# Kernel tuning notes

Hardware: AMD Instinct MI355X
Metric: run time of the kernel (lower is better)

## Reference

```python
import jax, jax.numpy as jnp
import numpy as np

NEG_SLOPE = 0.2


def _gat_layer(x, edge_index, W, a_src, a_dst, b):
    """PyG GATConv: linear -> per-edge attention logits -> segment softmax over
    destination -> scatter-add weighted messages. Self-loops added (PyG default)."""
    N = x.shape[0]
    heads, out = a_src.shape
    loops = jnp.arange(N, dtype=edge_index.dtype)
    src = jnp.concatenate([edge_index[0], loops])
    dst = jnp.concatenate([edge_index[1], loops])
    xh = (x @ W).reshape(N, heads, out)                      # [N,H,D]
    alpha_s = (xh * a_src).sum(-1)                           # [N,H]
    alpha_d = (xh * a_dst).sum(-1)                           # [N,H]
    e = jax.nn.leaky_relu(alpha_s[src] + alpha_d[dst], NEG_SLOPE)  # [E,H]
    emax = jax.ops.segment_max(e, dst, num_segments=N)       # [N,H]
    ex = jnp.exp(e - emax[dst])
    den = jax.ops.segment_sum(ex, dst, num_segments=N)
    att = ex / (den[dst] + 1e-16)                            # [E,H]
    msg = xh[src] * att[..., None]                           # [E,H,D]
    o = jax.ops.segment_sum(msg, dst, num_segments=N)        # [N,H,D]
    return o.reshape(N, heads * out) + b


def _single_source_gnn(h, edge_index, params):
    n_layers = len(params)
    for i, (W, a_s, a_d, b) in enumerate(params):
        h = _gat_layer(h, edge_index, W, a_s, a_d, b)
        if i < n_layers - 1:
            h = jax.nn.relu(h)
    return h


def setup_inputs() -> dict:
    key = jax.random.key(0)
    B, N, H, heads, deg = 4, 2000, 64, 4, 32
    E = N * deg
    ks = jax.random.split(key, 20)

    def mk_edge_index(k):
        e = jax.random.randint(k, (2, B, E), 0, N)
        off = (jnp.arange(B) * N)[None, :, None]
        return (e + off).reshape(2, B * E).astype(jnp.int32)

    inp = {
        "h0_flat": jax.random.normal(ks[0], (B * N, H), jnp.float32),
        "edge_index_s1": mk_edge_index(ks[1]),
        "edge_index_s2": mk_edge_index(ks[2]),
    }
    dims = [(H, H * heads), (H * heads, H * heads)]
    i = 3
    for s in ("s1", "s2"):
        for l, (din, dout) in enumerate(dims):
            inp[f"W_{s}_{l}"] = jax.random.normal(ks[i], (din, dout), jnp.float32) * 0.1; i += 1
            inp[f"a_src_{s}_{l}"] = jax.random.normal(ks[i], (heads, H), jnp.float32) * 0.1; i += 1
            inp[f"a_dst_{s}_{l}"] = jax.random.normal(ks[i], (heads, H), jnp.float32) * 0.1; i += 1
            inp[f"b_{s}_{l}"] = jnp.zeros((dout,), jnp.float32)
    inp["batch_size"] = B
    inp["num_stocks"] = N
    return inp


def reference(h0_flat, edge_index_s1, edge_index_s2,
              W_s1_0, a_src_s1_0, a_dst_s1_0, b_s1_0,
              W_s1_1, a_src_s1_1, a_dst_s1_1, b_s1_1,
              W_s2_0, a_src_s2_0, a_dst_s2_0, b_s2_0,
              W_s2_1, a_src_s2_1, a_dst_s2_1, b_s2_1,
              batch_size, num_stocks):
    p1 = [(W_s1_0, a_src_s1_0, a_dst_s1_0, b_s1_0),
          (W_s1_1, a_src_s1_1, a_dst_s1_1, b_s1_1)]
    p2 = [(W_s2_0, a_src_s2_0, a_dst_s2_0, b_s2_0),
          (W_s2_1, a_src_s2_1, a_dst_s2_1, b_s2_1)]
    h1 = _single_source_gnn(h0_flat, edge_index_s1, p1)
    h2 = _single_source_gnn(h0_flat, edge_index_s2, p2)
    # dict of per-source outputs in torch -> stacked [n_sources, B*N, H*heads]
    return jnp.stack([h1, h2])
```

## Files before the change

kernel.cpp:

```cpp
#include <hip/hip_runtime.h>
#include <hip/hip_fp16.h>


#define NEG_SLOPE 0.2f
#define ELLW 96
#define BK 64
#define HPAD 8

typedef _Float16 half8 __attribute__((ext_vector_type(8)));
typedef float floatx4 __attribute__((ext_vector_type(4)));

struct Args {
    const float* h0;
    const int *ei1, *ei2;
    const float *W10, *W11, *W20, *W21;
    const float *as10, *ad10, *b10, *as11, *ad11, *b11;
    const float *as20, *ad20, *b20, *as21, *ad21, *b21;
    _Float16 *Wt10, *Wt20, *Wt11, *Wt21;
    int *cnt, *slots;
    _Float16 *xh1, *xh2;
    _Float16 *hb1, *hb2;
    float *alS1, *alD1, *alS2, *alD2;
    float *out0, *out1;
    int N, E1, E2, GB0;
};


__global__ __launch_bounds__(64) void wt_zero_kernel(Args a) {
    int z = blockIdx.z, y = blockIdx.y, c = blockIdx.x;
    int t = threadIdx.x;
    int flat = ((z * gridDim.y + y) * gridDim.x + c) * 64 + t;
    if (flat < 2 * a.N) a.cnt[flat] = 0;
    if (y == 0) {
        const float* W  = z ? a.W20  : a.W10;
        _Float16*    Wt = z ? a.Wt20 : a.Wt10;
        Wt[(size_t)c * 64 + t] = (_Float16)W[(size_t)t * 256 + c];
    } else {
        int k = (y - 1) * 64 + t;
        const float* W  = z ? a.W21  : a.W11;
        _Float16*    Wt = z ? a.Wt21 : a.Wt11;
        Wt[(size_t)c * 256 + k] = (_Float16)W[(size_t)k * 256 + c];
    }
}


template<bool AHALF>
__device__ __forceinline__ void gemm_tile(
        const void* hv, const _Float16* __restrict__ Wt,
        const float* __restrict__ a_s, const float* __restrict__ a_d,
        _Float16* __restrict__ xh, float* __restrict__ alS,
        float* __restrict__ alD, int K, int row0,
        _Float16 (&hT)[32][BK + HPAD]) {
    int tid  = threadIdx.x;
    int wave = tid >> 6;
    int lane = tid & 63;
    int lo = lane & 15, hi = lane >> 4;
    int c0 = wave * 64;

    floatx4 acc[2][4] = {};

    int srow = tid >> 3, sseg = tid & 7;
    const _Float16* wbase = Wt + (size_t)c0 * K;

    for (int k0 = 0; k0 < K; k0 += BK) {
        __syncthreads();
        if (AHALF) {
            const _Float16* hrow = (const _Float16*)hv
                                 + (size_t)(row0 + srow) * K + sseg * 8;
            *(half8*)&hT[srow][sseg * 8] = *(const half8*)(hrow + k0);
        } else {
            const float* hrow = (const float*)hv
                              + (size_t)(row0 + srow) * K + sseg * 8;
            float4 hv0 = *(const float4*)(hrow + k0);
            float4 hv1 = *(const float4*)(hrow + k0 + 4);
            half8 hh;
            hh[0] = (_Float16)hv0.x; hh[1] = (_Float16)hv0.y;
            hh[2] = (_Float16)hv0.z; hh[3] = (_Float16)hv0.w;
            hh[4] = (_Float16)hv1.x; hh[5] = (_Float16)hv1.y;
            hh[6] = (_Float16)hv1.z; hh[7] = (_Float16)hv1.w;
            *(half8*)&hT[srow][sseg * 8] = hh;
        }
        __syncthreads();

        half8 bf[2][4], af[2][2];
#pragma unroll
        for (int ks = 0; ks < 2; ks++) {
#pragma unroll
            for (int cf = 0; cf < 4; cf++)
                bf[ks][cf] = *(const half8*)(wbase + (size_t)(cf * 16 + lo) * K
                                             + k0 + ks * 32 + hi * 8);
#pragma unroll
            for (int f = 0; f < 2; f++)
                af[ks][f] = *(const half8*)&hT[f * 16 + lo][ks * 32 + hi * 8];
        }
#pragma unroll
        for (int ks = 0; ks < 2; ks++)
#pragma unroll
            for (int f = 0; f < 2; f++)
#pragma unroll
                for (int cf = 0; cf < 4; cf++)
                    acc[f][cf] = __builtin_amdgcn_mfma_f32_16x16x32_f16(
                        af[ks][f], bf[ks][cf], acc[f][cf], 0, 0, 0);
    }

    float asw[4], adw[4];
#pragma unroll
    for (int cf = 0; cf < 4; cf++) {
        asw[cf] = a_s[c0 + cf * 16 + lo];
        adw[cf] = a_d[c0 + cf * 16 + lo];
    }
#pragma unroll
    for (int f = 0; f < 2; f++) {
#pragma unroll
        for (int r = 0; r < 4; r++) {
            int row = row0 + f * 16 + hi * 4 + r;
            float v0 = acc[f][0][r], v1 = acc[f][1][r];
            float v2 = acc[f][2][r], v3 = acc[f][3][r];
            _Float16* xrow = &xh[(size_t)row * 256 + c0 + lo];
            xrow[0]  = (_Float16)v0;
            xrow[16] = (_Float16)v1;
            xrow[32] = (_Float16)v2;
            xrow[48] = (_Float16)v3;
            float s1 = v0 * asw[0] + v1 * asw[1] + v2 * asw[2] + v3 * asw[3];
            float s2 = v0 * adw[0] + v1 * adw[1] + v2 * adw[2] + v3 * adw[3];
#pragma unroll
            for (int off = 1; off < 16; off <<= 1) {
                s1 += __shfl_xor(s1, off);
                s2 += __shfl_xor(s2, off);
            }
            if (lo == 0) {
                alS[row * 4 + wave] = s1;
                alD[row * 4 + wave] = s2;
            }
        }
    }
}


__global__ __launch_bounds__(256) void g0scat_kernel(Args a) {
    __shared__ _Float16 hT[32][BK + HPAD];
    int b = blockIdx.x;
    if (b < a.GB0) {
        int half_ = a.GB0 >> 1;
        int s = (b >= half_);
        int bx = b - s * half_;
        gemm_tile<false>(a.h0, s ? a.Wt20 : a.Wt10,
                         s ? a.as20 : a.as10, s ? a.ad20 : a.ad10,
                         s ? a.xh2 : a.xh1, s ? a.alS2 : a.alS1,
                         s ? a.alD2 : a.alD1, 64, bx * 32, hT);
    } else {
        int i = (b - a.GB0) * 256 + threadIdx.x;
        int tot1 = a.E1 + a.N, tot2 = a.E2 + a.N;
        if (i >= tot1 + tot2) return;
        int s, j; const int* ei; int E;
        if (i < tot1) { s = 0; j = i;        ei = a.ei1; E = a.E1; }
        else          { s = 1; j = i - tot1; ei = a.ei2; E = a.E2; }
        int src, dst;
        if (j < E) { src = ei[j]; dst = ei[E + j]; }
        else       { src = dst = j - E; }
        int gg = s * a.N + dst;
        int pos = atomicAdd(&a.cnt[gg], 1);
        if (pos < ELLW) a.slots[(size_t)gg * ELLW + pos] = src;
    }
}

__global__ __launch_bounds__(256) void gemm1_kernel(Args a) {
    __shared__ _Float16 hT[32][BK + HPAD];
    int half_ = a.GB0 >> 1;
    int b = blockIdx.x;
    int s = (b >= half_);
    int bx = b - s * half_;
    gemm_tile<true>(s ? a.hb2 : a.hb1, s ? a.Wt21 : a.Wt11,
                    s ? a.as21 : a.as11, s ? a.ad21 : a.ad11,
                    s ? a.xh2 : a.xh1, s ? a.alS2 : a.alS1,
                    s ? a.alD2 : a.alD1, 256, bx * 32, hT);
}


template<bool OUTHALF>
__device__ __forceinline__ void attn_impl(
        const Args& a, const float* __restrict__ b1, const float* __restrict__ b2,
        void* o1, void* o2, int do_relu) {
    __shared__ float2 pairs[4][8][10];
    int tid = threadIdx.x;
    int h = tid >> 6, L = tid & 63, st = L >> 3, lc = L & 7;
    int b = blockIdx.x;
    int cpx = (2 * a.N) >> 3;
    int g = (b & 7) * cpx + (b >> 3);
    int s = (g >= a.N) ? 1 : 0;
    int dst = g - s * a.N;
    const _Float16* xh  = s ? a.xh2  : a.xh1;
    const float*  alS   = s ? a.alS2 : a.alS1;
    const float*  alD   = s ? a.alD2 : a.alD1;
    const float*  bias  = s ? b2 : b1;
    void*         out   = s ? o2 : o1;

    const int* slots = a.slots + (size_t)g * ELLW;
    int pre = slots[L];
    int nd = a.cnt[g];
    if (nd > ELLW) nd = ELLW;
    float ad = alD[dst * 4 + h];
    const char* xb = (const char*)xh + h * 128 + lc * 16;

    float acc[8] = {};
    float pden = 0.f;

    for (int c = 0; c < nd; c += 64) {
        int n = nd - c; if (n > 64) n = 64;
        int off = 0; float p = 0.f;
        if (L < n) {
            int src = (c == 0) ? pre : slots[c + L];
            float t = alS[src * 4 + h] + ad;
            t = (t > 0.f) ? t : NEG_SLOPE * t;
            p = __expf(t);
            off = src * 512;
        }
        pden += p;
        pairs[h][L & 7][L >> 3] = make_float2(__int_as_float(off), p);
        int iters = (n + 7) >> 3;
        for (int ii = 0; ii < iters; ii += 4) {
            float4 twoA = *(const float4*)&pairs[h][st][ii];
            float4 twoB = *(const float4*)&pairs[h][st][ii + 2];
            int   o0 = __float_as_int(twoA.x); float w0 = twoA.y;
            int   o1i = __float_as_int(twoA.z); float w1 = twoA.w;
            int   o2i = __float_as_int(twoB.x); float w2 = twoB.y;
            int   o3i = __float_as_int(twoB.z); float w3 = twoB.w;
            float4 r0 = *(const float4*)(xb + o0);
            float4 r1 = *(const float4*)(xb + o1i);
            float4 r2 = *(const float4*)(xb + o2i);
            float4 r3 = *(const float4*)(xb + o3i);
            const __half2* q0 = (const __half2*)&r0;
            const __half2* q1 = (const __half2*)&r1;
            const __half2* q2 = (const __half2*)&r2;
            const __half2* q3 = (const __half2*)&r3;
#pragma unroll
            for (int k = 0; k < 4; k++) {
                acc[2 * k + 0] += (float)q0[k].x * w0;
                acc[2 * k + 1] += (float)q0[k].y * w0;
                acc[2 * k + 0] += (float)q1[k].x * w1;
                acc[2 * k + 1] += (float)q1[k].y * w1;
                acc[2 * k + 0] += (float)q2[k].x * w2;
                acc[2 * k + 1] += (float)q2[k].y * w2;
                acc[2 * k + 0] += (float)q3[k].x * w3;
                acc[2 * k + 1] += (float)q3[k].y * w3;
            }
        }
    }
#pragma unroll
    for (int k = 0; k < 8; k++) {
        acc[k] += __shfl_xor(acc[k], 8);
        acc[k] += __shfl_xor(acc[k], 16);
        acc[k] += __shfl_xor(acc[k], 32);
    }
#pragma unroll
    for (int o2_ = 32; o2_ >= 1; o2_ >>= 1) pden += __shfl_xor(pden, o2_);

    if (st == 0) {
        float d = 1.0f / (pden + 1e-16f);
        int col = h * 64 + lc * 8;
        float4 bA = *(const float4*)&bias[col];
        float4 bB = *(const float4*)&bias[col + 4];
        float o[8];
        o[0] = acc[0] * d + bA.x; o[1] = acc[1] * d + bA.y;
        o[2] = acc[2] * d + bA.z; o[3] = acc[3] * d + bA.w;
        o[4] = acc[4] * d + bB.x; o[5] = acc[5] * d + bB.y;
        o[6] = acc[6] * d + bB.z; o[7] = acc[7] * d + bB.w;
        if (do_relu) {
#pragma unroll
            for (int k = 0; k < 8; k++) o[k] = fmaxf(o[k], 0.f);
        }
        if (OUTHALF) {
            half8 ov;
#pragma unroll
            for (int k = 0; k < 8; k++) ov[k] = (_Float16)o[k];
            *(half8*)((_Float16*)out + (size_t)dst * 256 + col) = ov;
        } else {
            float4 oA, oB;
            oA.x = o[0]; oA.y = o[1]; oA.z = o[2]; oA.w = o[3];
            oB.x = o[4]; oB.y = o[5]; oB.z = o[6]; oB.w = o[7];
            *(float4*)((float*)out + (size_t)dst * 256 + col) = oA;
            *(float4*)((float*)out + (size_t)dst * 256 + col + 4) = oB;
        }
    }
}

__global__ __launch_bounds__(256) void attn0_kernel(Args a) {
    attn_impl<true>(a, a.b10, a.b20, a.hb1, a.hb2, 1);
}
__global__ __launch_bounds__(256) void attn1_kernel(Args a) {
    attn_impl<false>(a, a.b11, a.b21, a.out0, a.out1, 0);
}


extern "C" void kernel_launch(void* const* d_in, const int* in_sizes, int n_in,
                              void* d_out, int out_size, void* d_ws, size_t ws_size,
                              hipStream_t stream) {
    const int N  = in_sizes[0] / 64;
    const int E1 = in_sizes[1] / 2;
    const int E2 = in_sizes[2] / 2;

    char* base = (char*)d_ws;
    size_t off = 0;
    auto carve = [&](size_t bytes) -> void* {
        void* p = base + off;
        off += (bytes + 255) & ~(size_t)255;
        return p;
    };
    int* cnt        = (int*)carve((size_t)2 * N * 4);
    int* slots      = (int*)carve((size_t)2 * N * ELLW * 4);
    _Float16* xh1   = (_Float16*)carve((size_t)N * 256 * 2);
    _Float16* xh2   = (_Float16*)carve((size_t)N * 256 * 2);
    _Float16* hb1   = (_Float16*)carve((size_t)N * 256 * 2);
    _Float16* hb2   = (_Float16*)carve((size_t)N * 256 * 2);
    float* alS1     = (float*)carve((size_t)N * 4 * 4);
    float* alD1     = (float*)carve((size_t)N * 4 * 4);
    float* alS2     = (float*)carve((size_t)N * 4 * 4);
    float* alD2     = (float*)carve((size_t)N * 4 * 4);
    _Float16* Wt10  = (_Float16*)carve((size_t)256 * 64 * 2);
    _Float16* Wt20  = (_Float16*)carve((size_t)256 * 64 * 2);
    _Float16* Wt11  = (_Float16*)carve((size_t)256 * 256 * 2);
    _Float16* Wt21  = (_Float16*)carve((size_t)256 * 256 * 2);
    (void)ws_size; (void)n_in;

    Args a;
    a.h0 = (const float*)d_in[0];
    a.ei1 = (const int*)d_in[1];
    a.ei2 = (const int*)d_in[2];
    a.W10 = (const float*)d_in[3];  a.as10 = (const float*)d_in[4];
    a.ad10 = (const float*)d_in[5]; a.b10 = (const float*)d_in[6];
    a.W11 = (const float*)d_in[7];  a.as11 = (const float*)d_in[8];
    a.ad11 = (const float*)d_in[9]; a.b11 = (const float*)d_in[10];
    a.W20 = (const float*)d_in[11]; a.as20 = (const float*)d_in[12];
    a.ad20 = (const float*)d_in[13]; a.b20 = (const float*)d_in[14];
    a.W21 = (const float*)d_in[15]; a.as21 = (const float*)d_in[16];
    a.ad21 = (const float*)d_in[17]; a.b21 = (const float*)d_in[18];
    a.Wt10 = Wt10; a.Wt20 = Wt20; a.Wt11 = Wt11; a.Wt21 = Wt21;
    a.cnt = cnt; a.slots = slots;
    a.xh1 = xh1; a.xh2 = xh2; a.hb1 = hb1; a.hb2 = hb2;
    a.alS1 = alS1; a.alD1 = alD1; a.alS2 = alS2; a.alD2 = alD2;
    a.out0 = (float*)d_out; a.out1 = (float*)d_out + (size_t)N * 256;
    a.N = N; a.E1 = E1; a.E2 = E2;
    a.GB0 = (N / 32) * 2;

    int tot = (E1 + N) + (E2 + N);
    int scatterBlocks = (tot + 255) / 256;

    wt_zero_kernel<<<dim3(256, 5, 2), 64, 0, stream>>>(a);
    g0scat_kernel<<<a.GB0 + scatterBlocks, 256, 0, stream>>>(a);
    attn0_kernel<<<2 * N, 256, 0, stream>>>(a);
    gemm1_kernel<<<a.GB0, 256, 0, stream>>>(a);
    attn1_kernel<<<2 * N, 256, 0, stream>>>(a);
}
```

Baseline: 116.5 us.

## Aggregate raw features before layer-0 projection and fuse both GEMMs

Layer 0 is reordered so attention logits come from h0 dotted with precomputed W·a vectors, and the softmax-weighted aggregation gathers 64-wide fp16 h0 rows instead of 256-wide projected rows. The per-head aggregates are then projected by W0, given bias and ReLU, and fed straight through W1 in a single fused GEMM kernel with the intermediate kept in shared memory. This cuts gather traffic in the first attention pass and removes one kernel plus an intermediate global buffer. In exchange it adds an h0 fp16 conversion pass and redundant per-head aggregation, and rounding order changes slightly.

```diff
diff --git a/kernel.cpp b/kernel.cpp
--- a/kernel.cpp
+++ b/kernel.cpp
@@ -4,8 +4,6 @@
 
 #define NEG_SLOPE 0.2f
 #define ELLW 96
-#define BK 64
-#define HPAD 8
 
 typedef _Float16 half8 __attribute__((ext_vector_type(8)));
 typedef float floatx4 __attribute__((ext_vector_type(4)));
@@ -17,24 +15,40 @@
     const float *as10, *ad10, *b10, *as11, *ad11, *b11;
     const float *as20, *ad20, *b20, *as21, *ad21, *b21;
     _Float16 *Wt10, *Wt20, *Wt11, *Wt21;
+    float *vaS1, *vaD1, *vaS2, *vaD2;
+    _Float16 *h0h;
     int *cnt, *slots;
+    _Float16 *agg1, *agg2;
     _Float16 *xh1, *xh2;
-    _Float16 *hb1, *hb2;
     float *alS1, *alD1, *alS2, *alD2;
     float *out0, *out1;
-    int N, E1, E2, GB0;
+    int N, E1, E2, AB;
 };
 
 
-__global__ __launch_bounds__(64) void wt_zero_kernel(Args a) {
+__global__ __launch_bounds__(64) void prep_kernel(Args a) {
     int z = blockIdx.z, y = blockIdx.y, c = blockIdx.x;
     int t = threadIdx.x;
     int flat = ((z * gridDim.y + y) * gridDim.x + c) * 64 + t;
+    int GT = gridDim.x * gridDim.y * gridDim.z * 64;
     if (flat < 2 * a.N) a.cnt[flat] = 0;
+    for (int i = flat; i < a.N * 64; i += GT)
+        a.h0h[i] = (_Float16)a.h0[i];
     if (y == 0) {
         const float* W  = z ? a.W20  : a.W10;
         _Float16*    Wt = z ? a.Wt20 : a.Wt10;
         Wt[(size_t)c * 64 + t] = (_Float16)W[(size_t)t * 256 + c];
+        if (c < 8) {
+            int h = c & 3, sel = c >> 2;
+            const float* av = sel ? (z ? a.ad20 : a.ad10)
+                                  : (z ? a.as20 : a.as10);
+            float* va = sel ? (z ? a.vaD2 : a.vaD1)
+                            : (z ? a.vaS2 : a.vaS1);
+            float acc = 0.f;
+            for (int cc = 0; cc < 64; cc++)
+                acc += W[(size_t)t * 256 + h * 64 + cc] * av[h * 64 + cc];
+            va[h * 64 + t] = acc;
+        }
     } else {
         int k = (y - 1) * 64 + t;
         const float* W  = z ? a.W21  : a.W11;
@@ -44,112 +58,36 @@
 }
 
 
-template<bool AHALF>
-__device__ __forceinline__ void gemm_tile(
-        const void* hv, const _Float16* __restrict__ Wt,
-        const float* __restrict__ a_s, const float* __restrict__ a_d,
-        _Float16* __restrict__ xh, float* __restrict__ alS,
-        float* __restrict__ alD, int K, int row0,
-        _Float16 (&hT)[32][BK + HPAD]) {
-    int tid  = threadIdx.x;
-    int wave = tid >> 6;
-    int lane = tid & 63;
-    int lo = lane & 15, hi = lane >> 4;
-    int c0 = wave * 64;
-
-    floatx4 acc[2][4] = {};
-
-    int srow = tid >> 3, sseg = tid & 7;
-    const _Float16* wbase = Wt + (size_t)c0 * K;
-
-    for (int k0 = 0; k0 < K; k0 += BK) {
-        __syncthreads();
-        if (AHALF) {
-            const _Float16* hrow = (const _Float16*)hv
-                                 + (size_t)(row0 + srow) * K + sseg * 8;
-            *(half8*)&hT[srow][sseg * 8] = *(const half8*)(hrow + k0);
-        } else {
-            const float* hrow = (const float*)hv
-                              + (size_t)(row0 + srow) * K + sseg * 8;
-            float4 hv0 = *(const float4*)(hrow + k0);
-            float4 hv1 = *(const float4*)(hrow + k0 + 4);
-            half8 hh;
-            hh[0] = (_Float16)hv0.x; hh[1] = (_Float16)hv0.y;
-            hh[2] = (_Float16)hv0.z; hh[3] = (_Float16)hv0.w;
-            hh[4] = (_Float16)hv1.x; hh[5] = (_Float16)hv1.y;
-            hh[6] = (_Float16)hv1.z; hh[7] = (_Float16)hv1.w;
-            *(half8*)&hT[srow][sseg * 8] = hh;
-        }
-        __syncthreads();
-
-        half8 bf[2][4], af[2][2];
-#pragma unroll
-        for (int ks = 0; ks < 2; ks++) {
-#pragma unroll
-            for (int cf = 0; cf < 4; cf++)
-                bf[ks][cf] = *(const half8*)(wbase + (size_t)(cf * 16 + lo) * K
-                                             + k0 + ks * 32 + hi * 8);
-#pragma unroll
-            for (int f = 0; f < 2; f++)
-                af[ks][f] = *(const half8*)&hT[f * 16 + lo][ks * 32 + hi * 8];
-        }
-#pragma unroll
-        for (int ks = 0; ks < 2; ks++)
-#pragma unroll
-            for (int f = 0; f < 2; f++)
-#pragma unroll
-                for (int cf = 0; cf < 4; cf++)
-                    acc[f][cf] = __builtin_amdgcn_mfma_f32_16x16x32_f16(
-                        af[ks][f], bf[ks][cf], acc[f][cf], 0, 0, 0);
-    }
-
-    float asw[4], adw[4];
-#pragma unroll
-    for (int cf = 0; cf < 4; cf++) {
-        asw[cf] = a_s[c0 + cf * 16 + lo];
-        adw[cf] = a_d[c0 + cf * 16 + lo];
-    }
-#pragma unroll
-    for (int f = 0; f < 2; f++) {
-#pragma unroll
-        for (int r = 0; r < 4; r++) {
-            int row = row0 + f * 16 + hi * 4 + r;
-            float v0 = acc[f][0][r], v1 = acc[f][1][r];
-            float v2 = acc[f][2][r], v3 = acc[f][3][r];
-            _Float16* xrow = &xh[(size_t)row * 256 + c0 + lo];
-            xrow[0]  = (_Float16)v0;
-            xrow[16] = (_Float16)v1;
-            xrow[32] = (_Float16)v2;
-            xrow[48] = (_Float16)v3;
-            float s1 = v0 * asw[0] + v1 * asw[1] + v2 * asw[2] + v3 * asw[3];
-            float s2 = v0 * adw[0] + v1 * adw[1] + v2 * adw[2] + v3 * adw[3];
-#pragma unroll
-            for (int off = 1; off < 16; off <<= 1) {
-                s1 += __shfl_xor(s1, off);
-                s2 += __shfl_xor(s2, off);
-            }
-            if (lo == 0) {
-                alS[row * 4 + wave] = s1;
-                alD[row * 4 + wave] = s2;
-            }
-        }
-    }
-}
-
-
-__global__ __launch_bounds__(256) void g0scat_kernel(Args a) {
-    __shared__ _Float16 hT[32][BK + HPAD];
+__global__ __launch_bounds__(256) void scat_al0_kernel(Args a) {
     int b = blockIdx.x;
-    if (b < a.GB0) {
-        int half_ = a.GB0 >> 1;
-        int s = (b >= half_);
-        int bx = b - s * half_;
-        gemm_tile<false>(a.h0, s ? a.Wt20 : a.Wt10,
-                         s ? a.as20 : a.as10, s ? a.ad20 : a.ad10,
-                         s ? a.xh2 : a.xh1, s ? a.alS2 : a.alS1,
-                         s ? a.alD2 : a.alD1, 64, bx * 32, hT);
+    int tid = threadIdx.x;
+    if (b < a.AB) {
+        int g = b * 4 + (tid >> 6);
+        if (g >= 2 * a.N) return;
+        int L = tid & 63;
+        int s = (g >= a.N) ? 1 : 0;
+        int i = g - s * a.N;
+        const float* vaS = s ? a.vaS2 : a.vaS1;
+        const float* vaD = s ? a.vaD2 : a.vaD1;
+        float* alS = s ? a.alS2 : a.alS1;
+        float* alD = s ? a.alD2 : a.alD1;
+        float x = a.h0[(size_t)i * 64 + L];
+#pragma unroll
+        for (int h = 0; h < 4; h++) {
+            float sv = x * vaS[h * 64 + L];
+            float dv = x * vaD[h * 64 + L];
+#pragma unroll
+            for (int off = 32; off >= 1; off >>= 1) {
+                sv += __shfl_xor(sv, off);
+                dv += __shfl_xor(dv, off);
+            }
+            if (L == 0) {
+                alS[i * 4 + h] = sv;
+                alD[i * 4 + h] = dv;
+            }
+        }
     } else {
-        int i = (b - a.GB0) * 256 + threadIdx.x;
+        int i = (b - a.AB) * 256 + tid;
         int tot1 = a.E1 + a.N, tot2 = a.E2 + a.N;
         if (i >= tot1 + tot2) return;
         int s, j; const int* ei; int E;
@@ -164,23 +102,8 @@
     }
 }
 
-__global__ __launch_bounds__(256) void gemm1_kernel(Args a) {
-    __shared__ _Float16 hT[32][BK + HPAD];
-    int half_ = a.GB0 >> 1;
-    int b = blockIdx.x;
-    int s = (b >= half_);
-    int bx = b - s * half_;
-    gemm_tile<true>(s ? a.hb2 : a.hb1, s ? a.Wt21 : a.Wt11,
-                    s ? a.as21 : a.as11, s ? a.ad21 : a.ad11,
-                    s ? a.xh2 : a.xh1, s ? a.alS2 : a.alS1,
-                    s ? a.alD2 : a.alD1, 256, bx * 32, hT);
-}
-
-
-template<bool OUTHALF>
-__device__ __forceinline__ void attn_impl(
-        const Args& a, const float* __restrict__ b1, const float* __restrict__ b2,
-        void* o1, void* o2, int do_relu) {
+
+__global__ __launch_bounds__(256) void attn_agg_kernel(Args a) {
     __shared__ float2 pairs[4][8][10];
     int tid = threadIdx.x;
     int h = tid >> 6, L = tid & 63, st = L >> 3, lc = L & 7;
@@ -189,18 +112,16 @@
     int g = (b & 7) * cpx + (b >> 3);
     int s = (g >= a.N) ? 1 : 0;
     int dst = g - s * a.N;
-    const _Float16* xh  = s ? a.xh2  : a.xh1;
-    const float*  alS   = s ? a.alS2 : a.alS1;
-    const float*  alD   = s ? a.alD2 : a.alD1;
-    const float*  bias  = s ? b2 : b1;
-    void*         out   = s ? o2 : o1;
+    const float* alS = s ? a.alS2 : a.alS1;
+    const float* alD = s ? a.alD2 : a.alD1;
+    _Float16*    agg = s ? a.agg2 : a.agg1;
 
     const int* slots = a.slots + (size_t)g * ELLW;
     int pre = slots[L];
     int nd = a.cnt[g];
     if (nd > ELLW) nd = ELLW;
     float ad = alD[dst * 4 + h];
-    const char* xb = (const char*)xh + h * 128 + lc * 16;
+    const char* xb = (const char*)a.h0h + lc * 16;
 
     float acc[8] = {};
     float pden = 0.f;
@@ -213,7 +134,7 @@
             float t = alS[src * 4 + h] + ad;
             t = (t > 0.f) ? t : NEG_SLOPE * t;
             p = __expf(t);
-            off = src * 512;
+            off = src * 128;
         }
         pden += p;
         pairs[h][L & 7][L >> 3] = make_float2(__int_as_float(off), p);
@@ -258,37 +179,215 @@
     if (st == 0) {
         float d = 1.0f / (pden + 1e-16f);
         int col = h * 64 + lc * 8;
+        half8 ov;
+#pragma unroll
+        for (int k = 0; k < 8; k++) ov[k] = (_Float16)(acc[k] * d);
+        *(half8*)(agg + (size_t)dst * 256 + col) = ov;
+    }
+}
+
+
+__global__ __launch_bounds__(256) void fusedgemm_kernel(Args a) {
+    __shared__ _Float16 hT[32][264];
+    int half_ = (a.N / 32);
+    int b = blockIdx.x;
+    int s = (b >= half_);
+    int bx = b - s * half_;
+    int row0 = bx * 32;
+
+    const _Float16* agg = s ? a.agg2 : a.agg1;
+    const _Float16* Wt0 = s ? a.Wt20 : a.Wt10;
+    const _Float16* Wt1 = s ? a.Wt21 : a.Wt11;
+    const float* bias0  = s ? a.b20  : a.b10;
+    const float* a_s    = s ? a.as21 : a.as11;
+    const float* a_d    = s ? a.ad21 : a.ad11;
+    _Float16* xh = s ? a.xh2 : a.xh1;
+    float* alS = s ? a.alS2 : a.alS1;
+    float* alD = s ? a.alD2 : a.alD1;
+
+    int tid  = threadIdx.x;
+    int wave = tid >> 6;
+    int lane = tid & 63;
+    int lo = lane & 15, hi = lane >> 4;
+    int c0 = wave * 64;
+
+    {
+        floatx4 acc[2][4] = {};
+#pragma unroll
+        for (int ks = 0; ks < 2; ks++) {
+            half8 af[2], bf[4];
+#pragma unroll
+            for (int f = 0; f < 2; f++)
+                af[f] = *(const half8*)(agg + (size_t)(row0 + f * 16 + lo) * 256
+                                        + c0 + ks * 32 + hi * 8);
+#pragma unroll
+            for (int cf = 0; cf < 4; cf++)
+                bf[cf] = *(const half8*)(Wt0 + (size_t)(c0 + cf * 16 + lo) * 64
+                                         + ks * 32 + hi * 8);
+#pragma unroll
+            for (int f = 0; f < 2; f++)
+#pragma unroll
+                for (int cf = 0; cf < 4; cf++)
+                    acc[f][cf] = __builtin_amdgcn_mfma_f32_16x16x32_f16(
+                        af[f], bf[cf], acc[f][cf], 0, 0, 0);
+        }
+        float bb[4];
+#pragma unroll
+        for (int cf = 0; cf < 4; cf++) bb[cf] = bias0[c0 + cf * 16 + lo];
+#pragma unroll
+        for (int f = 0; f < 2; f++)
+#pragma unroll
+            for (int cf = 0; cf < 4; cf++)
+#pragma unroll
+                for (int r = 0; r < 4; r++) {
+                    int row = f * 16 + hi * 4 + r;
+                    float v = acc[f][cf][r] + bb[cf];
+                    hT[row][c0 + cf * 16 + lo] = (_Float16)fmaxf(v, 0.f);
+                }
+    }
+    __syncthreads();
+
+    floatx4 acc[2][4] = {};
+#pragma unroll
+    for (int ks = 0; ks < 8; ks++) {
+        half8 af[2], bf[4];
+#pragma unroll
+        for (int f = 0; f < 2; f++)
+            af[f] = *(const half8*)&hT[f * 16 + lo][ks * 32 + hi * 8];
+#pragma unroll
+        for (int cf = 0; cf < 4; cf++)
+            bf[cf] = *(const half8*)(Wt1 + (size_t)(c0 + cf * 16 + lo) * 256
+                                     + ks * 32 + hi * 8);
+#pragma unroll
+        for (int f = 0; f < 2; f++)
+#pragma unroll
+            for (int cf = 0; cf < 4; cf++)
+                acc[f][cf] = __builtin_amdgcn_mfma_f32_16x16x32_f16(
+                    af[f], bf[cf], acc[f][cf], 0, 0, 0);
+    }
+
+    float asw[4], adw[4];
+#pragma unroll
+    for (int cf = 0; cf < 4; cf++) {
+        asw[cf] = a_s[c0 + cf * 16 + lo];
+        adw[cf] = a_d[c0 + cf * 16 + lo];
+    }
+#pragma unroll
+    for (int f = 0; f < 2; f++) {
+#pragma unroll
+        for (int r = 0; r < 4; r++) {
+            int row = row0 + f * 16 + hi * 4 + r;
+            float v0 = acc[f][0][r], v1 = acc[f][1][r];
+            float v2 = acc[f][2][r], v3 = acc[f][3][r];
+            _Float16* xrow = &xh[(size_t)row * 256 + c0 + lo];
+            xrow[0]  = (_Float16)v0;
+            xrow[16] = (_Float16)v1;
+            xrow[32] = (_Float16)v2;
+            xrow[48] = (_Float16)v3;
+            float s1 = v0 * asw[0] + v1 * asw[1] + v2 * asw[2] + v3 * asw[3];
+            float s2 = v0 * adw[0] + v1 * adw[1] + v2 * adw[2] + v3 * adw[3];
+#pragma unroll
+            for (int off = 1; off < 16; off <<= 1) {
+                s1 += __shfl_xor(s1, off);
+                s2 += __shfl_xor(s2, off);
+            }
+            if (lo == 0) {
+                alS[row * 4 + wave] = s1;
+                alD[row * 4 + wave] = s2;
+            }
+        }
+    }
+}
+
+
+__global__ __launch_bounds__(256) void attn1_kernel(Args a) {
+    __shared__ float2 pairs[4][8][10];
+    int tid = threadIdx.x;
+    int h = tid >> 6, L = tid & 63, st = L >> 3, lc = L & 7;
+    int b = blockIdx.x;
+    int cpx = (2 * a.N) >> 3;
+    int g = (b & 7) * cpx + (b >> 3);
+    int s = (g >= a.N) ? 1 : 0;
+    int dst = g - s * a.N;
+    const _Float16* xh = s ? a.xh2  : a.xh1;
+    const float* alS   = s ? a.alS2 : a.alS1;
+    const float* alD   = s ? a.alD2 : a.alD1;
+    const float* bias  = s ? a.b21  : a.b11;
+    float* out         = s ? a.out1 : a.out0;
+
+    const int* slots = a.slots + (size_t)g * ELLW;
+    int pre = slots[L];
+    int nd = a.cnt[g];
+    if (nd > ELLW) nd = ELLW;
+    float ad = alD[dst * 4 + h];
+    const char* xb = (const char*)xh + h * 128 + lc * 16;
+
+    float acc[8] = {};
+    float pden = 0.f;
+
+    for (int c = 0; c < nd; c += 64) {
+        int n = nd - c; if (n > 64) n = 64;
+        int off = 0; float p = 0.f;
+        if (L < n) {
+            int src = (c == 0) ? pre : slots[c + L];
+            float t = alS[src * 4 + h] + ad;
+            t = (t > 0.f) ? t : NEG_SLOPE * t;
+            p = __expf(t);
+            off = src * 512;
+        }
+        pden += p;
+        pairs[h][L & 7][L >> 3] = make_float2(__int_as_float(off), p);
+        int iters = (n + 7) >> 3;
+        for (int ii = 0; ii < iters; ii += 4) {
+            float4 twoA = *(const float4*)&pairs[h][st][ii];
+            float4 twoB = *(const float4*)&pairs[h][st][ii + 2];
+            int   o0 = __float_as_int(twoA.x); float w0 = twoA.y;
+            int   o1i = __float_as_int(twoA.z); float w1 = twoA.w;
+            int   o2i = __float_as_int(twoB.x); float w2 = twoB.y;
+            int   o3i = __float_as_int(twoB.z); float w3 = twoB.w;
+            float4 r0 = *(const float4*)(xb + o0);
+            float4 r1 = *(const float4*)(xb + o1i);
+            float4 r2 = *(const float4*)(xb + o2i);
+            float4 r3 = *(const float4*)(xb + o3i);
+            const __half2* q0 = (const __half2*)&r0;
+            const __half2* q1 = (const __half2*)&r1;
+            const __half2* q2 = (const __half2*)&r2;
+            const __half2* q3 = (const __half2*)&r3;
+#pragma unroll
+            for (int k = 0; k < 4; k++) {
+                acc[2 * k + 0] += (float)q0[k].x * w0;
+                acc[2 * k + 1] += (float)q0[k].y * w0;
+                acc[2 * k + 0] += (float)q1[k].x * w1;
+                acc[2 * k + 1] += (float)q1[k].y * w1;
+                acc[2 * k + 0] += (float)q2[k].x * w2;
+                acc[2 * k + 1] += (float)q2[k].y * w2;
+                acc[2 * k + 0] += (float)q3[k].x * w3;
+                acc[2 * k + 1] += (float)q3[k].y * w3;
+            }
+        }
+    }
+#pragma unroll
+    for (int k = 0; k < 8; k++) {
+        acc[k] += __shfl_xor(acc[k], 8);
+        acc[k] += __shfl_xor(acc[k], 16);
+        acc[k] += __shfl_xor(acc[k], 32);
+    }
+#pragma unroll
+    for (int o2_ = 32; o2_ >= 1; o2_ >>= 1) pden += __shfl_xor(pden, o2_);
+
+    if (st == 0) {
+        float d = 1.0f / (pden + 1e-16f);
+        int col = h * 64 + lc * 8;
         float4 bA = *(const float4*)&bias[col];
         float4 bB = *(const float4*)&bias[col + 4];
-        float o[8];
-        o[0] = acc[0] * d + bA.x; o[1] = acc[1] * d + bA.y;
-        o[2] = acc[2] * d + bA.z; o[3] = acc[3] * d + bA.w;
-        o[4] = acc[4] * d + bB.x; o[5] = acc[5] * d + bB.y;
-        o[6] = acc[6] * d + bB.z; o[7] = acc[7] * d + bB.w;
-        if (do_relu) {
-#pragma unroll
-            for (int k = 0; k < 8; k++) o[k] = fmaxf(o[k], 0.f);
-        }
-        if (OUTHALF) {
-            half8 ov;
-#pragma unroll
-            for (int k = 0; k < 8; k++) ov[k] = (_Float16)o[k];
-            *(half8*)((_Float16*)out + (size_t)dst * 256 + col) = ov;
-        } else {
-            float4 oA, oB;
-            oA.x = o[0]; oA.y = o[1]; oA.z = o[2]; oA.w = o[3];
-            oB.x = o[4]; oB.y = o[5]; oB.z = o[6]; oB.w = o[7];
-            *(float4*)((float*)out + (size_t)dst * 256 + col) = oA;
-            *(float4*)((float*)out + (size_t)dst * 256 + col + 4) = oB;
-        }
-    }
-}
-
-__global__ __launch_bounds__(256) void attn0_kernel(Args a) {
-    attn_impl<true>(a, a.b10, a.b20, a.hb1, a.hb2, 1);
-}
-__global__ __launch_bounds__(256) void attn1_kernel(Args a) {
-    attn_impl<false>(a, a.b11, a.b21, a.out0, a.out1, 0);
+        float4 oA, oB;
+        oA.x = acc[0] * d + bA.x; oA.y = acc[1] * d + bA.y;
+        oA.z = acc[2] * d + bA.z; oA.w = acc[3] * d + bA.w;
+        oB.x = acc[4] * d + bB.x; oB.y = acc[5] * d + bB.y;
+        oB.z = acc[6] * d + bB.z; oB.w = acc[7] * d + bB.w;
+        *(float4*)&out[(size_t)dst * 256 + col] = oA;
+        *(float4*)&out[(size_t)dst * 256 + col + 4] = oB;
+    }
 }
 
 
@@ -308,10 +407,10 @@
     };
     int* cnt        = (int*)carve((size_t)2 * N * 4);
     int* slots      = (int*)carve((size_t)2 * N * ELLW * 4);
+    _Float16* agg1  = (_Float16*)carve((size_t)N * 256 * 2);
+    _Float16* agg2  = (_Float16*)carve((size_t)N * 256 * 2);
     _Float16* xh1   = (_Float16*)carve((size_t)N * 256 * 2);
     _Float16* xh2   = (_Float16*)carve((size_t)N * 256 * 2);
-    _Float16* hb1   = (_Float16*)carve((size_t)N * 256 * 2);
-    _Float16* hb2   = (_Float16*)carve((size_t)N * 256 * 2);
     float* alS1     = (float*)carve((size_t)N * 4 * 4);
     float* alD1     = (float*)carve((size_t)N * 4 * 4);
     float* alS2     = (float*)carve((size_t)N * 4 * 4);
@@ -320,6 +419,11 @@
     _Float16* Wt20  = (_Float16*)carve((size_t)256 * 64 * 2);
     _Float16* Wt11  = (_Float16*)carve((size_t)256 * 256 * 2);
     _Float16* Wt21  = (_Float16*)carve((size_t)256 * 256 * 2);
+    float* vaS1     = (float*)carve((size_t)256 * 4);
+    float* vaD1     = (float*)carve((size_t)256 * 4);
+    float* vaS2     = (float*)carve((size_t)256 * 4);
+    float* vaD2     = (float*)carve((size_t)256 * 4);
+    _Float16* h0h   = (_Float16*)carve((size_t)N * 64 * 2);
     (void)ws_size; (void)n_in;
 
     Args a;
@@ -335,19 +439,22 @@
     a.W21 = (const float*)d_in[15]; a.as21 = (const float*)d_in[16];
     a.ad21 = (const float*)d_in[17]; a.b21 = (const float*)d_in[18];
     a.Wt10 = Wt10; a.Wt20 = Wt20; a.Wt11 = Wt11; a.Wt21 = Wt21;
+    a.vaS1 = vaS1; a.vaD1 = vaD1; a.vaS2 = vaS2; a.vaD2 = vaD2;
+    a.h0h = h0h;
     a.cnt = cnt; a.slots = slots;
-    a.xh1 = xh1; a.xh2 = xh2; a.hb1 = hb1; a.hb2 = hb2;
+    a.agg1 = agg1; a.agg2 = agg2;
+    a.xh1 = xh1; a.xh2 = xh2;
     a.alS1 = alS1; a.alD1 = alD1; a.alS2 = alS2; a.alD2 = alD2;
     a.out0 = (float*)d_out; a.out1 = (float*)d_out + (size_t)N * 256;
     a.N = N; a.E1 = E1; a.E2 = E2;
-    a.GB0 = (N / 32) * 2;
+    a.AB = (2 * N + 3) / 4;
 
     int tot = (E1 + N) + (E2 + N);
     int scatterBlocks = (tot + 255) / 256;
 
-    wt_zero_kernel<<<dim3(256, 5, 2), 64, 0, stream>>>(a);
-    g0scat_kernel<<<a.GB0 + scatterBlocks, 256, 0, stream>>>(a);
-    attn0_kernel<<<2 * N, 256, 0, stream>>>(a);
-    gemm1_kernel<<<a.GB0, 256, 0, stream>>>(a);
+    prep_kernel<<<dim3(256, 5, 2), 64, 0, stream>>>(a);
+    scat_al0_kernel<<<a.AB + scatterBlocks, 256, 0, stream>>>(a);
+    attn_agg_kernel<<<2 * N, 256, 0, stream>>>(a);
+    fusedgemm_kernel<<<(N / 32) * 2, 256, 0, stream>>>(a);
     attn1_kernel<<<2 * N, 256, 0, stream>>>(a);
 }
```

After: 120.1 us. 3.1% more time.
